# Optimization experiments

Hardware: AMD Instinct MI355X
Metric: run time of the kernel (lower is better)

Reference implementation:

```python
import jax, jax.numpy as jnp
import numpy as np

B, C, H, W = 8, 1024, 56, 56
NBINS = 256          # torch.histc(bins=256, min=0, max=1)
T_THRESH = 0.9       # EKLM entropy-ratio threshold
NUM_CLASSES = 30


def setup_inputs() -> dict:
    key = jax.random.key(0)
    k1, k2 = jax.random.split(key)
    x = jax.random.uniform(k1, (B, C, H, W), dtype=jnp.float32)
    w_fc = jax.random.normal(k2, (C, NUM_CLASSES), dtype=jnp.float32) * 0.02
    return {"x": x, "w_fc": w_fc}


def _integral_hist(x):
    """One fused pass replacing the per-region torch.histc calls.
    Returns per-(h,w)-cell histograms [H,W,256] and their 2D inclusive
    prefix sum padded to [H+1,W+1,256] so any rectangle histogram is 4 lookups.
    Matches torch.histc semantics: values outside [0,1] ignored, v==1 -> last bin."""
    valid = (x >= 0.0) & (x <= 1.0)
    q = jnp.clip(jnp.floor(x * NBINS), 0, NBINS - 1).astype(jnp.int32)
    q = jnp.where(valid, q, NBINS)  # out-of-range -> extra bin, dropped below
    hh = jnp.broadcast_to(jnp.arange(H)[None, None, :, None], x.shape)
    ww = jnp.broadcast_to(jnp.arange(W)[None, None, None, :], x.shape)
    cell = jnp.zeros((H, W, NBINS + 1), jnp.float32).at[hh, ww, q].add(1.0)[..., :NBINS]
    integ = jnp.cumsum(jnp.cumsum(cell, axis=0), axis=1)
    integ = jnp.pad(integ, ((1, 0), (1, 0), (0, 0)))  # [H+1, W+1, 256]
    return cell, integ


def _entropy_of_hist(h):
    p = h / jnp.sum(h)
    return -jnp.sum(p * jnp.log2(p + 1e-9))


def _region_entropy(integ, xs, xd, ys, yd):
    # histogram of x[:, :, xs:xd, ys:yd] via integral-histogram lookups
    h = integ[xd, yd] - integ[xs, yd] - integ[xd, ys] + integ[xs, ys]
    return _entropy_of_hist(h)


def eklm(x):
    """Entropy-based Key Localization Method (xs fixed to 0, as in source)."""
    cell, integ = _integral_hist(x)
    # compute_entropy_for_each_y: entropy of each [:, :, 0:1, y:y+1] column cell
    col_hists = cell[0]  # [W, 256]
    p = col_hists / jnp.sum(col_hists, axis=1, keepdims=True)
    ent_y = -jnp.sum(p * jnp.log2(p + 1e-9), axis=1)
    ys0 = jnp.argmax(ent_y).astype(jnp.int32)
    total_ent = _region_entropy(integ, 0, H, 0, W)

    def ent(xd, ys, yd):
        return _region_entropy(integ, 0, xd, ys, yd)

    def cond(state):
        xd, ys, yd, Ts, done = state
        return (Ts < T_THRESH) & (~done)

    def body(state):
        xd, ys, yd, Ts, done = state
        e_cur = ent(xd, ys, yd)
        # greedy priority identical to source: grow xd, else shrink ys, else grow yd
        c1 = (xd + 1 < H) & (ent(xd + 1, ys, yd) > e_cur)
        c2 = (~c1) & (ys - 1 >= 0) & (ent(xd, jnp.maximum(ys - 1, 0), yd) > e_cur)
        c3 = (~c1) & (~c2) & (yd + 1 < W) & (ent(xd, ys, jnp.minimum(yd + 1, W)) > e_cur)
        xd_n = jnp.where(c1, xd + 1, xd)
        ys_n = jnp.where(c2, ys - 1, ys)
        yd_n = jnp.where(c3, yd + 1, yd)
        done_n = ~(c1 | c2 | c3)
        Ts_n = ent(xd_n, ys_n, yd_n) / total_ent
        return (xd_n, ys_n, yd_n, Ts_n, done_n)

    xd0 = jnp.int32(1)
    yd0 = ys0 + jnp.int32(1)
    Ts0 = ent(xd0, ys0, yd0) / total_ent
    xd, ys, yd, _, _ = jax.lax.while_loop(
        cond, body, (xd0, ys0, yd0, Ts0, jnp.bool_(False)))
    return jnp.int32(0), xd, ys, yd


def reference(x, w_fc):
    xs, xd, ys, yd = eklm(x)
    # crop the located key region (mask form for static shapes), mean-pool, classify
    row = jnp.arange(H)
    col = jnp.arange(W)
    mask = ((row[:, None] >= xs) & (row[:, None] < xd)
            & (col[None, :] >= ys) & (col[None, :] < yd)).astype(x.dtype)
    area = jnp.maximum(jnp.sum(mask), 1.0)
    pooled = jnp.einsum('bchw,hw->bc', x, mask) / area  # [B, C]
    return pooled @ w_fc  # [B, NUM_CLASSES]
```

## Files before the change

### kernel.cpp

```cpp
#include <hip/hip_runtime.h>
#include <hip/hip_cooperative_groups.h>
#include <math.h>

namespace cg = cooperative_groups;

#define BB 8
#define CC 1024
#define HH 56
#define WW 56
#define NB 256
#define NCLS 30
#define BC (BB * CC)
#define PLANE (HH * WW)
#define NWORD (NB / 2)
#define CELLW (PLANE * NWORD)
#define SLICES 16
#define PL_PER_SLICE (BC / SLICES)

#define NPART 16
#define GH_BLOCKS 3136
#define F4_PER_BLOCK 2048

#define FULL_NEED 28934400ull

__global__ void zero_kernel(unsigned* __restrict__ p) {
    p[blockIdx.x * 256 + threadIdx.x] = 0u;
}

__global__ __launch_bounds__(256) void ghist_kernel(const float* __restrict__ x,
                                                    unsigned* __restrict__ gpart) {
    __shared__ unsigned lh[4 * NB];
    const int tid = threadIdx.x;
    lh[tid] = 0u; lh[NB + tid] = 0u; lh[2 * NB + tid] = 0u; lh[3 * NB + tid] = 0u;
    __syncthreads();

    const float4* __restrict__ xb =
        (const float4*)x + (size_t)blockIdx.x * F4_PER_BLOCK;
    float4 v[8];
#pragma unroll
    for (int it = 0; it < 8; ++it) v[it] = xb[it * 256 + tid];

    unsigned* wl = lh + ((tid >> 6) << 8);
#pragma unroll
    for (int it = 0; it < 8; ++it) {
        const float vv[4] = {v[it].x, v[it].y, v[it].z, v[it].w};
#pragma unroll
        for (int e = 0; e < 4; ++e) {
            const float f = vv[e];
            if (f >= 0.f && f <= 1.f) {
                int bin = (int)(f * 256.f);
                if (bin > 255) bin = 255;
                atomicAdd(&wl[bin], 1u);
            }
        }
    }
    __syncthreads();
    const unsigned s = lh[tid] + lh[NB + tid] + lh[2 * NB + tid] + lh[3 * NB + tid];
    if (s) atomicAdd(&gpart[((blockIdx.x & (NPART - 1)) << 8) + tid], s);
}

__global__ __launch_bounds__(256) void colhist_kernel(const float* __restrict__ x,
                                                      unsigned* __restrict__ colhist) {
    __shared__ unsigned ch[HH * NWORD];
    const int tid = threadIdx.x;
    for (int i = tid; i < HH * NWORD; i += 256) ch[i] = 0u;
    __syncthreads();

    const float* __restrict__ xb = x + (size_t)blockIdx.x * 32 * PLANE;
    for (int j = tid; j < 32 * 14; j += 256) {
        const int pl = j / 14;
        const int wq = j - pl * 14;
        const float4 v = *(const float4*)(xb + (size_t)pl * PLANE + wq * 4);
        const float vv[4] = {v.x, v.y, v.z, v.w};
#pragma unroll
        for (int e = 0; e < 4; ++e) {
            const float f = vv[e];
            if (f >= 0.f && f <= 1.f) {
                int bin = (int)(f * 256.f);
                if (bin > 255) bin = 255;
                atomicAdd(&ch[(wq * 4 + e) * NWORD + (bin >> 1)],
                          1u << ((bin & 1) << 4));
            }
        }
    }
    __syncthreads();
    for (int i = tid; i < HH * NWORD; i += 256) {
        const unsigned v = ch[i];
        if (v) atomicAdd(&colhist[i], v);
    }
}

__device__ __forceinline__ float wave_sum(float v) {
#pragma unroll
    for (int off = 32; off > 0; off >>= 1) v += __shfl_xor(v, off);
    return v;
}

__device__ __forceinline__ float ilook(const unsigned* __restrict__ integ,
                                       int a, int b, int bin) {
    return (a == 0 || b == 0)
               ? 0.f
               : (float)integ[((size_t)((a - 1) * WW + (b - 1))) * NB + bin];
}

__device__ float region_ent(const unsigned* __restrict__ integ, int lane,
                            int xd, int ys, int yd) {
    float hb[4];
    float hs = 0.f;
#pragma unroll
    for (int k = 0; k < 4; k++) {
        const int bin = lane + 64 * k;
        const float hv = ilook(integ, xd, yd, bin) - ilook(integ, xd, ys, bin);
        hb[k] = hv;
        hs += hv;
    }
    hs = wave_sum(hs);
    float e = 0.f;
#pragma unroll
    for (int k = 0; k < 4; k++) {
        const float p = hb[k] / hs;
        e += p * log2f(p + 1e-9f);
    }
    return -wave_sum(e);
}

__global__ __launch_bounds__(1024) void decide_fast_kernel(
    const unsigned* __restrict__ colhist, const unsigned* __restrict__ gpart,
    int* __restrict__ region, unsigned* __restrict__ flag) {
    __shared__ float ent_s[WW];
    const int tid = threadIdx.x;
    const int lane = tid & 63;
    const int wv = tid >> 6;

    for (int w = wv; w < WW; w += 16) {
        float hb[4], hs = 0.f;
#pragma unroll
        for (int k = 0; k < 4; k++) {
            const int bin = lane + 64 * k;
            const unsigned wd = colhist[w * NWORD + (bin >> 1)];
            hb[k] = (float)((wd >> ((bin & 1) << 4)) & 0xffffu);
            hs += hb[k];
        }
        hs = wave_sum(hs);
        float e = 0.f;
#pragma unroll
        for (int k = 0; k < 4; k++) {
            const float p = hb[k] / hs;
            e += p * log2f(p + 1e-9f);
        }
        e = -wave_sum(e);
        if (lane == 0) ent_s[w] = e;
    }
    __syncthreads();
    if (wv != 0) return;

    float best = -3.0e38f;
    int bestw = 0;
    for (int w = 0; w < WW; ++w) {
        const float e = ent_s[w];
        if (e > best) { best = e; bestw = w; }
    }

    float hb[4], hs = 0.f;
#pragma unroll
    for (int k = 0; k < 4; k++) {
        const int bin = lane + 64 * k;
        unsigned t = 0;
#pragma unroll
        for (int p = 0; p < NPART; ++p) t += gpart[(p << 8) + bin];
        hb[k] = (float)t;
        hs += hb[k];
    }
    hs = wave_sum(hs);
    float e = 0.f;
#pragma unroll
    for (int k = 0; k < 4; k++) {
        const float p = hb[k] / hs;
        e += p * log2f(p + 1e-9f);
    }
    const float total_ent = -wave_sum(e);

    const float Ts0 = best / total_ent;
    if (lane == 0) {
        region[0] = 1;
        region[1] = bestw;
        region[2] = bestw + 1;
        *flag = (Ts0 >= 0.9f) ? 1u : 2u;
    }
}

__global__ __launch_bounds__(256) void fallback_kernel(
    const float* __restrict__ x, unsigned* __restrict__ ps,
    unsigned* __restrict__ hist, int* __restrict__ region,
    const unsigned* __restrict__ flag) {
    if (*flag == 1u) return;
    cg::grid_group grid = cg::this_grid();
    __shared__ unsigned lh[HH * NWORD];
    const int tid = threadIdx.x;
    const int gtid = blockIdx.x * 256 + tid;

    for (int t = blockIdx.x; t < HH * SLICES; t += 256) {
        const int h = t % HH;
        const int slice = t / HH;
        for (int i = tid; i < HH * NWORD; i += 256) lh[i] = 0u;
        __syncthreads();
        const float* __restrict__ xb =
            x + (size_t)(slice * PL_PER_SLICE) * PLANE + h * WW;
        for (int it = 0; it < 28; ++it) {
            const int j = it * 256 + tid;
            const int bcl = j / 14;
            const int wq = j - bcl * 14;
            const float4 v = *(const float4*)(xb + (size_t)bcl * PLANE + wq * 4);
            const float vv[4] = {v.x, v.y, v.z, v.w};
#pragma unroll
            for (int e = 0; e < 4; ++e) {
                const float f = vv[e];
                if (f >= 0.f && f <= 1.f) {
                    int bin = (int)(f * 256.f);
                    if (bin > 255) bin = 255;
                    atomicAdd(&lh[(wq * 4 + e) * NWORD + (bin >> 1)],
                              1u << ((bin & 1) << 4));
                }
            }
        }
        __syncthreads();
        unsigned* g = ps + (size_t)slice * CELLW + (size_t)h * WW * NWORD;
        for (int i = tid; i < HH * NWORD; i += 256) g[i] = lh[i];
        __syncthreads();
    }
    grid.sync();

    for (int idx = gtid; idx < CELLW; idx += 256 * 256) {
        unsigned s = 0;
#pragma unroll
        for (int sl = 0; sl < SLICES; ++sl) s += ps[(size_t)sl * CELLW + idx];
        ((uint2*)hist)[idx] = make_uint2(s & 0xffffu, s >> 16);
    }
    grid.sync();

    if (gtid < HH * NB) {
        const int h = gtid >> 8, b = gtid & 255;
        unsigned* base = hist + (size_t)h * WW * NB + b;
        unsigned v[WW];
#pragma unroll
        for (int w = 0; w < WW; ++w) v[w] = base[(size_t)w * NB];
        unsigned c = 0;
#pragma unroll
        for (int w = 0; w < WW; ++w) { c += v[w]; base[(size_t)w * NB] = c; }
    }
    grid.sync();

    if (gtid < WW * NB) {
        const int w = gtid >> 8, b = gtid & 255;
        unsigned* base = hist + (size_t)w * NB + b;
        unsigned v[HH];
#pragma unroll
        for (int h = 0; h < HH; ++h) v[h] = base[(size_t)h * WW * NB];
        unsigned c = 0;
#pragma unroll
        for (int h = 0; h < HH; ++h) { c += v[h]; base[(size_t)h * WW * NB] = c; }
    }
    grid.sync();

    if (blockIdx.x == 0 && tid < 64) {
        const int lane = tid;
        const float total_ent = region_ent(hist, lane, HH, 0, WW);
        int xd = region[0], ys = region[1], yd = region[2];
        float Ts = region_ent(hist, lane, xd, ys, yd) / total_ent;
        bool done = false;
        int iter = 0;
        while (Ts < 0.9f && !done && iter < 1000) {
            iter++;
            const float e_cur = region_ent(hist, lane, xd, ys, yd);
            const int ysm = (ys - 1 < 0) ? 0 : ys - 1;
            const int ydp = (yd + 1 > WW) ? WW : yd + 1;
            const bool c1 = (xd + 1 < HH) &&
                            (region_ent(hist, lane, xd + 1, ys, yd) > e_cur);
            const bool c2 = !c1 && (ys - 1 >= 0) &&
                            (region_ent(hist, lane, xd, ysm, yd) > e_cur);
            const bool c3 = !c1 && !c2 && (yd + 1 < WW) &&
                            (region_ent(hist, lane, xd, ys, ydp) > e_cur);
            if (c1) xd = xd + 1;
            else if (c2) ys = ys - 1;
            else if (c3) yd = yd + 1;
            done = !(c1 || c2 || c3);
            Ts = region_ent(hist, lane, xd, ys, yd) / total_ent;
        }
        if (lane == 0) {
            region[0] = xd;
            region[1] = ys;
            region[2] = yd;
        }
    }
}

__global__ __launch_bounds__(256) void pool_kernel(const float* __restrict__ x,
                                                   const int* __restrict__ region,
                                                   float* __restrict__ pooled) {
    const int xd = region[0], ys = region[1], yd = region[2];
    const int Wd = yd - ys;
    const int n = xd * Wd;
    const float area = fmaxf((float)n, 1.f);
    if (n <= 16) {
        const int bc = blockIdx.x * 256 + threadIdx.x;
        const float* plane = x + (size_t)bc * PLANE;
        float s = 0.f;
        for (int j = 0; j < n; ++j) {
            const int r = j / Wd;
            const int cc = ys + (j - r * Wd);
            s += plane[r * WW + cc];
        }
        pooled[bc] = s / area;
    } else {
        const int wid = (blockIdx.x * 256 + threadIdx.x) >> 6;
        const int lane = threadIdx.x & 63;
        for (int bc = wid; bc < BC; bc += 128) {
            const float* plane = x + (size_t)bc * PLANE;
            float s = 0.f;
            for (int j = lane; j < n; j += 64) {
                const int r = j / Wd;
                const int cc = ys + (j - r * Wd);
                s += plane[r * WW + cc];
            }
#pragma unroll
            for (int off = 32; off > 0; off >>= 1) s += __shfl_xor(s, off);
            if (lane == 0) pooled[bc] = s / area;
        }
    }
}

__global__ __launch_bounds__(256) void fc_kernel(const float* __restrict__ pooled,
                                                 const float* __restrict__ wfc,
                                                 float* __restrict__ out) {
    __shared__ float red[240];
    const int b = blockIdx.x;
    const int t = threadIdx.x;
    if (t < 240) {
        const int chunk = t / NCLS;
        const int n = t - chunk * NCLS;
        const float* pv = pooled + b * CC + chunk * 128;
        const float* wv = wfc + (size_t)(chunk * 128) * NCLS + n;
        float a0 = 0.f, a1 = 0.f, a2 = 0.f, a3 = 0.f;
        for (int c = 0; c < 128; c += 4) {
            a0 += pv[c + 0] * wv[(c + 0) * NCLS];
            a1 += pv[c + 1] * wv[(c + 1) * NCLS];
            a2 += pv[c + 2] * wv[(c + 2) * NCLS];
            a3 += pv[c + 3] * wv[(c + 3) * NCLS];
        }
        red[t] = (a0 + a1) + (a2 + a3);
    }
    __syncthreads();
    if (t < NCLS) {
        float s = 0.f;
#pragma unroll
        for (int ch = 0; ch < 8; ++ch) s += red[ch * NCLS + t];
        out[b * NCLS + t] = s;
    }
}

extern "C" void kernel_launch(void* const* d_in, const int* in_sizes, int n_in,
                              void* d_out, int out_size, void* d_ws, size_t ws_size,
                              hipStream_t stream) {
    const float* x = (const float*)d_in[0];
    const float* wfc = (const float*)d_in[1];
    float* out = (float*)d_out;

    unsigned char* ws = (unsigned char*)d_ws;
    const bool full = (ws_size >= FULL_NEED);

    unsigned* colhist = (unsigned*)ws;
    unsigned* gpart = (unsigned*)(ws + HH * NWORD * 4);
    unsigned* ps = (unsigned*)ws;
    unsigned* hist = (unsigned*)(ws + (size_t)SLICES * CELLW * 4);
    int* region;
    unsigned* flag;
    float* pooled;
    if (full) {
        unsigned char* meta = ws + 28901376ull;
        region = (int*)meta;
        flag = (unsigned*)(meta + 16);
        pooled = (float*)(ws + 28901632ull);
    } else {
        region = (int*)(ws + 46080);
        flag = (unsigned*)(ws + 46080 + 16);
        pooled = (float*)(ws + 47104);
    }

    zero_kernel<<<44, 256, 0, stream>>>(colhist);
    ghist_kernel<<<GH_BLOCKS, 256, 0, stream>>>(x, gpart);
    colhist_kernel<<<256, 256, 0, stream>>>(x, colhist);
    decide_fast_kernel<<<1, 1024, 0, stream>>>(colhist, gpart, region, flag);
    if (full) {
        const float* xx = x;
        unsigned* psp = ps;
        unsigned* hp = hist;
        int* rp = region;
        unsigned* fp = flag;
        void* kargs[] = {(void*)&xx, (void*)&psp, (void*)&hp, (void*)&rp,
                         (void*)&fp};
        hipLaunchCooperativeKernel((const void*)fallback_kernel, dim3(256),
                                   dim3(256), kargs, 0, stream);
    }
    pool_kernel<<<32, 256, 0, stream>>>(x, region, pooled);
    fc_kernel<<<BB, 256, 0, stream>>>(pooled, wfc, out);
}
```

Before: 202.8 us.

## Fuse column histogram into global pass, replace cooperative launch, merge pool into FC

Result: faster. 169.8 us (-16.3%).

```diff
diff --git a/kernel.cpp b/kernel.cpp
--- a/kernel.cpp
+++ b/kernel.cpp
@@ -1,8 +1,5 @@
 #include <hip/hip_runtime.h>
-#include <hip/hip_cooperative_groups.h>
 #include <math.h>
-
-namespace cg = cooperative_groups;
 
 #define BB 8
 #define CC 1024
@@ -20,22 +17,26 @@
 #define NPART 16
 #define GH_BLOCKS 3136
 #define F4_PER_BLOCK 2048
+#define FB_BLOCKS 256
 
 #define FULL_NEED 28934400ull
-
-__global__ void zero_kernel(unsigned* __restrict__ p) {
+#define META_OFF 28901376ull
+
+__global__ void zero_kernel(unsigned* __restrict__ p, unsigned* __restrict__ bar) {
     p[blockIdx.x * 256 + threadIdx.x] = 0u;
+    if (blockIdx.x == 0 && threadIdx.x < 8) bar[threadIdx.x] = 0u;
 }
 
 __global__ __launch_bounds__(256) void ghist_kernel(const float* __restrict__ x,
+                                                    unsigned* __restrict__ colhist,
                                                     unsigned* __restrict__ gpart) {
     __shared__ unsigned lh[4 * NB];
     const int tid = threadIdx.x;
     lh[tid] = 0u; lh[NB + tid] = 0u; lh[2 * NB + tid] = 0u; lh[3 * NB + tid] = 0u;
     __syncthreads();
 
-    const float4* __restrict__ xb =
-        (const float4*)x + (size_t)blockIdx.x * F4_PER_BLOCK;
+    const size_t base_f4 = (size_t)blockIdx.x * F4_PER_BLOCK;
+    const float4* __restrict__ xb = (const float4*)x + base_f4;
     float4 v[8];
 #pragma unroll
     for (int it = 0; it < 8; ++it) v[it] = xb[it * 256 + tid];
@@ -43,6 +44,11 @@
     unsigned* wl = lh + ((tid >> 6) << 8);
 #pragma unroll
     for (int it = 0; it < 8; ++it) {
+        const int j = it * 256 + tid;
+        const int e0 = ((int)base_f4 + j) * 4;
+        const int pl = e0 / PLANE;
+        const int li = e0 - pl * PLANE;
+        const bool r0 = (li < WW);
         const float vv[4] = {v[it].x, v[it].y, v[it].z, v[it].w};
 #pragma unroll
         for (int e = 0; e < 4; ++e) {
@@ -51,43 +57,13 @@
                 int bin = (int)(f * 256.f);
                 if (bin > 255) bin = 255;
                 atomicAdd(&wl[bin], 1u);
+                if (r0) atomicAdd(&colhist[(li + e) * NB + bin], 1u);
             }
         }
     }
     __syncthreads();
     const unsigned s = lh[tid] + lh[NB + tid] + lh[2 * NB + tid] + lh[3 * NB + tid];
     if (s) atomicAdd(&gpart[((blockIdx.x & (NPART - 1)) << 8) + tid], s);
-}
-
-__global__ __launch_bounds__(256) void colhist_kernel(const float* __restrict__ x,
-                                                      unsigned* __restrict__ colhist) {
-    __shared__ unsigned ch[HH * NWORD];
-    const int tid = threadIdx.x;
-    for (int i = tid; i < HH * NWORD; i += 256) ch[i] = 0u;
-    __syncthreads();
-
-    const float* __restrict__ xb = x + (size_t)blockIdx.x * 32 * PLANE;
-    for (int j = tid; j < 32 * 14; j += 256) {
-        const int pl = j / 14;
-        const int wq = j - pl * 14;
-        const float4 v = *(const float4*)(xb + (size_t)pl * PLANE + wq * 4);
-        const float vv[4] = {v.x, v.y, v.z, v.w};
-#pragma unroll
-        for (int e = 0; e < 4; ++e) {
-            const float f = vv[e];
-            if (f >= 0.f && f <= 1.f) {
-                int bin = (int)(f * 256.f);
-                if (bin > 255) bin = 255;
-                atomicAdd(&ch[(wq * 4 + e) * NWORD + (bin >> 1)],
-                          1u << ((bin & 1) << 4));
-            }
-        }
-    }
-    __syncthreads();
-    for (int i = tid; i < HH * NWORD; i += 256) {
-        const unsigned v = ch[i];
-        if (v) atomicAdd(&colhist[i], v);
-    }
 }
 
 __device__ __forceinline__ float wave_sum(float v) {
@@ -137,8 +113,7 @@
 #pragma unroll
         for (int k = 0; k < 4; k++) {
             const int bin = lane + 64 * k;
-            const unsigned wd = colhist[w * NWORD + (bin >> 1)];
-            hb[k] = (float)((wd >> ((bin & 1) << 4)) & 0xffffu);
+            hb[k] = (float)colhist[w * NB + bin];
             hs += hb[k];
         }
         hs = wave_sum(hs);
@@ -189,17 +164,30 @@
     }
 }
 
+__device__ __forceinline__ void soft_grid_sync(unsigned* __restrict__ bar,
+                                               int idx, unsigned nb) {
+    __syncthreads();
+    if (threadIdx.x == 0) {
+        __threadfence();
+        atomicAdd(&bar[idx], 1u);
+        while (atomicAdd(&bar[idx], 0u) < nb) {
+            __builtin_amdgcn_s_sleep(8);
+        }
+    }
+    __syncthreads();
+    __threadfence();
+}
+
 __global__ __launch_bounds__(256) void fallback_kernel(
     const float* __restrict__ x, unsigned* __restrict__ ps,
     unsigned* __restrict__ hist, int* __restrict__ region,
-    const unsigned* __restrict__ flag) {
+    const unsigned* __restrict__ flag, unsigned* __restrict__ bar) {
     if (*flag == 1u) return;
-    cg::grid_group grid = cg::this_grid();
     __shared__ unsigned lh[HH * NWORD];
     const int tid = threadIdx.x;
     const int gtid = blockIdx.x * 256 + tid;
 
-    for (int t = blockIdx.x; t < HH * SLICES; t += 256) {
+    for (int t = blockIdx.x; t < HH * SLICES; t += FB_BLOCKS) {
         const int h = t % HH;
         const int slice = t / HH;
         for (int i = tid; i < HH * NWORD; i += 256) lh[i] = 0u;
@@ -228,15 +216,15 @@
         for (int i = tid; i < HH * NWORD; i += 256) g[i] = lh[i];
         __syncthreads();
     }
-    grid.sync();
-
-    for (int idx = gtid; idx < CELLW; idx += 256 * 256) {
+    soft_grid_sync(bar, 0, FB_BLOCKS);
+
+    for (int idx = gtid; idx < CELLW; idx += FB_BLOCKS * 256) {
         unsigned s = 0;
 #pragma unroll
         for (int sl = 0; sl < SLICES; ++sl) s += ps[(size_t)sl * CELLW + idx];
         ((uint2*)hist)[idx] = make_uint2(s & 0xffffu, s >> 16);
     }
-    grid.sync();
+    soft_grid_sync(bar, 1, FB_BLOCKS);
 
     if (gtid < HH * NB) {
         const int h = gtid >> 8, b = gtid & 255;
@@ -248,7 +236,7 @@
 #pragma unroll
         for (int w = 0; w < WW; ++w) { c += v[w]; base[(size_t)w * NB] = c; }
     }
-    grid.sync();
+    soft_grid_sync(bar, 2, FB_BLOCKS);
 
     if (gtid < WW * NB) {
         const int w = gtid >> 8, b = gtid & 255;
@@ -260,7 +248,7 @@
 #pragma unroll
         for (int h = 0; h < HH; ++h) { c += v[h]; base[(size_t)h * WW * NB] = c; }
     }
-    grid.sync();
+    soft_grid_sync(bar, 3, FB_BLOCKS);
 
     if (blockIdx.x == 0 && tid < 64) {
         const int lane = tid;
@@ -294,52 +282,37 @@
     }
 }
 
-__global__ __launch_bounds__(256) void pool_kernel(const float* __restrict__ x,
-                                                   const int* __restrict__ region,
-                                                   float* __restrict__ pooled) {
+__global__ __launch_bounds__(256) void fc_kernel(const float* __restrict__ x,
+                                                 const int* __restrict__ region,
+                                                 const float* __restrict__ wfc,
+                                                 float* __restrict__ out) {
+    __shared__ float pl_s[CC];
+    __shared__ float red[240];
+    const int b = blockIdx.x;
+    const int t = threadIdx.x;
     const int xd = region[0], ys = region[1], yd = region[2];
     const int Wd = yd - ys;
     const int n = xd * Wd;
     const float area = fmaxf((float)n, 1.f);
-    if (n <= 16) {
-        const int bc = blockIdx.x * 256 + threadIdx.x;
-        const float* plane = x + (size_t)bc * PLANE;
+    const float* __restrict__ xb = x + (size_t)b * CC * PLANE;
+#pragma unroll
+    for (int k = 0; k < 4; ++k) {
+        const int c = t + k * 256;
+        const float* plane = xb + (size_t)c * PLANE;
         float s = 0.f;
         for (int j = 0; j < n; ++j) {
             const int r = j / Wd;
-            const int cc = ys + (j - r * Wd);
-            s += plane[r * WW + cc];
-        }
-        pooled[bc] = s / area;
-    } else {
-        const int wid = (blockIdx.x * 256 + threadIdx.x) >> 6;
-        const int lane = threadIdx.x & 63;
-        for (int bc = wid; bc < BC; bc += 128) {
-            const float* plane = x + (size_t)bc * PLANE;
-            float s = 0.f;
-            for (int j = lane; j < n; j += 64) {
-                const int r = j / Wd;
-                const int cc = ys + (j - r * Wd);
-                s += plane[r * WW + cc];
-            }
-#pragma unroll
-            for (int off = 32; off > 0; off >>= 1) s += __shfl_xor(s, off);
-            if (lane == 0) pooled[bc] = s / area;
-        }
-    }
-}
-
-__global__ __launch_bounds__(256) void fc_kernel(const float* __restrict__ pooled,
-                                                 const float* __restrict__ wfc,
-                                                 float* __restrict__ out) {
-    __shared__ float red[240];
-    const int b = blockIdx.x;
-    const int t = threadIdx.x;
+            const int cc2 = ys + (j - r * Wd);
+            s += plane[r * WW + cc2];
+        }
+        pl_s[c] = s / area;
+    }
+    __syncthreads();
     if (t < 240) {
         const int chunk = t / NCLS;
-        const int n = t - chunk * NCLS;
-        const float* pv = pooled + b * CC + chunk * 128;
-        const float* wv = wfc + (size_t)(chunk * 128) * NCLS + n;
+        const int nn = t - chunk * NCLS;
+        const float* pv = pl_s + chunk * 128;
+        const float* wv = wfc + (size_t)(chunk * 128) * NCLS + nn;
         float a0 = 0.f, a1 = 0.f, a2 = 0.f, a3 = 0.f;
         for (int c = 0; c < 128; c += 4) {
             a0 += pv[c + 0] * wv[(c + 0) * NCLS];
@@ -369,38 +342,29 @@
     const bool full = (ws_size >= FULL_NEED);
 
     unsigned* colhist = (unsigned*)ws;
-    unsigned* gpart = (unsigned*)(ws + HH * NWORD * 4);
+    unsigned* gpart = (unsigned*)(ws + 57344);
     unsigned* ps = (unsigned*)ws;
     unsigned* hist = (unsigned*)(ws + (size_t)SLICES * CELLW * 4);
     int* region;
     unsigned* flag;
-    float* pooled;
+    unsigned* bar;
     if (full) {
-        unsigned char* meta = ws + 28901376ull;
+        unsigned char* meta = ws + META_OFF;
         region = (int*)meta;
         flag = (unsigned*)(meta + 16);
-        pooled = (float*)(ws + 28901632ull);
+        bar = (unsigned*)(meta + 32);
     } else {
-        region = (int*)(ws + 46080);
-        flag = (unsigned*)(ws + 46080 + 16);
-        pooled = (float*)(ws + 47104);
-    }
-
-    zero_kernel<<<44, 256, 0, stream>>>(colhist);
-    ghist_kernel<<<GH_BLOCKS, 256, 0, stream>>>(x, gpart);
-    colhist_kernel<<<256, 256, 0, stream>>>(x, colhist);
+        region = (int*)(ws + 73728);
+        flag = (unsigned*)(ws + 73728 + 16);
+        bar = (unsigned*)(ws + 73728 + 32);
+    }
+
+    zero_kernel<<<72, 256, 0, stream>>>(colhist, bar);
+    ghist_kernel<<<GH_BLOCKS, 256, 0, stream>>>(x, colhist, gpart);
     decide_fast_kernel<<<1, 1024, 0, stream>>>(colhist, gpart, region, flag);
     if (full) {
-        const float* xx = x;
-        unsigned* psp = ps;
-        unsigned* hp = hist;
-        int* rp = region;
-        unsigned* fp = flag;
-        void* kargs[] = {(void*)&xx, (void*)&psp, (void*)&hp, (void*)&rp,
-                         (void*)&fp};
-        hipLaunchCooperativeKernel((const void*)fallback_kernel, dim3(256),
-                                   dim3(256), kargs, 0, stream);
-    }
-    pool_kernel<<<32, 256, 0, stream>>>(x, region, pooled);
-    fc_kernel<<<BB, 256, 0, stream>>>(pooled, wfc, out);
-}
+        fallback_kernel<<<FB_BLOCKS, 256, 0, stream>>>(x, ps, hist, region,
+                                                       flag, bar);
+    }
+    fc_kernel<<<BB, 256, 0, stream>>>(x, region, wfc, out);
+}
```
